# Performance work log

Measured on AMD Instinct MI355X. Metric: run time of the kernel, lower is better.

The kernel has to match this reference:

```python
import jax, jax.numpy as jnp
import numpy as np

IN_CH, OUT_CH = 256, 128
HID = 2 * OUT_CH  # 256
N_NODES, N_EDGES = 50000, 800000


def setup_inputs() -> dict:
    key = jax.random.key(0)
    k1, k2, k3, k4, k5, k6, k7 = jax.random.split(key, 7)
    feats = jax.random.normal(k1, (N_NODES, IN_CH), dtype=jnp.float32)
    src = jax.random.randint(k2, (N_EDGES,), 0, N_NODES, dtype=jnp.int64)
    dst = jax.random.randint(k3, (N_EDGES,), 0, N_NODES, dtype=jnp.int64)
    # GraphConv weights: layer0 in->2*out, layer1 2*out->out (Glorot-ish scale)
    W0 = jax.random.normal(k4, (IN_CH, HID), dtype=jnp.float32) / np.sqrt(IN_CH)
    b0 = jnp.zeros((HID,), dtype=jnp.float32)
    W1 = jax.random.normal(k5, (HID, OUT_CH), dtype=jnp.float32) / np.sqrt(HID)
    b1 = jnp.zeros((OUT_CH,), dtype=jnp.float32)
    return {"feats": feats, "src": src, "dst": dst, "W0": W0, "b0": b0, "W1": W1, "b1": b1}


def _graph_conv(x, W, b, src, dst, norm_src, norm_dst, n_nodes):
    # Apply W first (out <= in) to shrink the edge-gather intermediate, as DGL does.
    h = x @ W                                  # [N, out]
    h = h * norm_src[:, None]                  # D_src^-1/2
    msg = h[src]                               # [E, out] irregular gather
    agg = jax.ops.segment_sum(msg, dst, num_segments=n_nodes)  # SpMM
    agg = agg * norm_dst[:, None] + b          # D_dst^-1/2, bias
    return jax.nn.relu(agg)


def reference(feats, src, dst, W0, b0, W1, b1):
    n = feats.shape[0]
    loop = jnp.arange(n, dtype=src.dtype)
    src_sl = jnp.concatenate([src, loop])      # dgl.add_self_loop
    dst_sl = jnpp = jnp.concatenate([dst, loop])
    ones = jnp.ones_like(src_sl, dtype=feats.dtype)
    out_deg = jax.ops.segment_sum(ones, src_sl, num_segments=n)
    in_deg = jax.ops.segment_sum(ones, dst_sl, num_segments=n)
    norm_src = jax.lax.rsqrt(jnp.maximum(out_deg, 1.0))
    norm_dst = jax.lax.rsqrt(jnp.maximum(in_deg, 1.0))
    x = _graph_conv(feats, W0, b0, src_sl, dst_sl, norm_src, norm_dst, n)
    x = _graph_conv(x, W1, b1, src_sl, dst_sl, norm_src, norm_dst, n)
    return x
```

## Files before the change

kernel.cpp:

```cpp
#include <hip/hip_runtime.h>


typedef __attribute__((ext_vector_type(8))) short short8v;
typedef __attribute__((ext_vector_type(4))) float float4v;
typedef __attribute__((ext_vector_type(8))) _Float16 half8v;
typedef __attribute__((ext_vector_type(4))) _Float16 half4v;
typedef __attribute__((ext_vector_type(2))) _Float16 half2v;

__device__ inline unsigned short f2bf(float x) {
  unsigned u = __float_as_uint(x);
  return (unsigned short)((u + 0x7FFFu + ((u >> 16) & 1u)) >> 16);
}
__device__ inline float bf2f(unsigned short b) {
  return __uint_as_float(((unsigned)b) << 16);
}

__global__ __launch_bounds__(256) void k_hist8(const int* __restrict__ src,
                                               const int* __restrict__ dst,
                                               unsigned* __restrict__ cnt,
                                               int N, int E) {
  unsigned xcc;
  asm("s_getreg_b32 %0, hwreg(HW_REG_XCC_ID)" : "=s"(xcc));
  unsigned* my = cnt + (size_t)(xcc & 7) * 2u * (unsigned)N;
  int base = blockIdx.x * 1024 + threadIdx.x;
  int s4[4], d4[4];
  bool ok[4];
#pragma unroll
  for (int i = 0; i < 4; ++i) {
    int e = base + i * 256;
    ok[i] = e < E;
    if (ok[i]) { s4[i] = src[e]; d4[i] = dst[e]; }
  }
#pragma unroll
  for (int i = 0; i < 4; ++i) {
    if (ok[i]) {
      __hip_atomic_fetch_add(&my[s4[i]], 1u, __ATOMIC_RELAXED,
                             __HIP_MEMORY_SCOPE_WORKGROUP);
      __hip_atomic_fetch_add(&my[N + d4[i]], 1u, __ATOMIC_RELAXED,
                             __HIP_MEMORY_SCOPE_WORKGROUP);
    }
  }
}

__global__ __launch_bounds__(256) void k_scan1_norm(
    const unsigned* __restrict__ cnt, int* __restrict__ part,
    int* __restrict__ bsums, float* __restrict__ nsrc,
    float* __restrict__ ndst, int N) {
  __shared__ int s[256];
  int t = threadIdx.x, g = blockIdx.x * 256 + t;
  int od = 0, id = 0;
  if (g < N) {
#pragma unroll
    for (int x = 0; x < 8; ++x) {
      od += cnt[(size_t)x * 2u * (unsigned)N + g];
      id += cnt[(size_t)x * 2u * (unsigned)N + N + g];
    }
    nsrc[g] = rsqrtf((float)(od + 1));
    ndst[g] = rsqrtf((float)(id + 1));
  }
  int v = (g < N) ? id : 0;
  s[t] = v;
  __syncthreads();
  for (int o = 1; o < 256; o <<= 1) {
    int add = (t >= o) ? s[t - o] : 0;
    __syncthreads();
    s[t] += add;
    __syncthreads();
  }
  if (g < N) part[g] = s[t] - v;
  if (t == 255) bsums[blockIdx.x] = s[255];
}

__global__ __launch_bounds__(256) void k_scan23(
    int* __restrict__ part, int* __restrict__ cursor8,
    const int* __restrict__ bsums, const unsigned* __restrict__ cnt,
    int nb, int N, int E) {
  __shared__ int s[256];
  int t = threadIdx.x, g = blockIdx.x * 256 + t;
  int v = (t < nb) ? bsums[t] : 0;
  s[t] = v;
  __syncthreads();
  for (int o = 1; o < 256; o <<= 1) {
    int add = (t >= o) ? s[t - o] : 0;
    __syncthreads();
    s[t] += add;
    __syncthreads();
  }
  int off = s[blockIdx.x] - bsums[blockIdx.x];
  if (g < N) {
    int r = part[g] + off;
    part[g] = r;
    int run = r;
#pragma unroll
    for (int x = 0; x < 8; ++x) {
      cursor8[(size_t)x * N + g] = run;
      run += cnt[(size_t)x * 2u * (unsigned)N + N + g];
    }
  }
  if (g == 0) part[N] = E;
}

__global__ __launch_bounds__(256) void k_fill8(const int* __restrict__ src,
                                               const int* __restrict__ dst,
                                               int* __restrict__ cursor8,
                                               int* __restrict__ colidx,
                                               int N, int E) {
  unsigned xcc;
  asm("s_getreg_b32 %0, hwreg(HW_REG_XCC_ID)" : "=s"(xcc));
  int* my = cursor8 + (size_t)(xcc & 7) * N;
  int base = blockIdx.x * 1024 + threadIdx.x;
  int s4[4], d4[4];
  bool ok[4];
#pragma unroll
  for (int i = 0; i < 4; ++i) {
    int e = base + i * 256;
    ok[i] = e < E;
    if (ok[i]) { s4[i] = src[e]; d4[i] = dst[e]; }
  }
  int p4[4];
#pragma unroll
  for (int i = 0; i < 4; ++i) {
    if (ok[i])
      p4[i] = __hip_atomic_fetch_add(&my[d4[i]], 1, __ATOMIC_RELAXED,
                                     __HIP_MEMORY_SCOPE_WORKGROUP);
  }
#pragma unroll
  for (int i = 0; i < 4; ++i) {
    if (ok[i]) colidx[p4[i]] = s4[i];
  }
}

__global__ __launch_bounds__(256) void k_wsplit2(
    const float* __restrict__ W0, short* __restrict__ W0tH,
    short* __restrict__ W0tL, const float* __restrict__ W1,
    short* __restrict__ W1tH, short* __restrict__ W1tL) {
  const int K = 256, N0 = 256, N1 = 128;
  int idx = blockIdx.x * 256 + threadIdx.x;
  if (idx < K * N0) {
    int k = idx & (K - 1), n = idx >> 8;
    float v = W0[(size_t)k * N0 + n];
    unsigned short h = f2bf(v);
    W0tH[(size_t)n * K + k] = (short)h;
    W0tL[(size_t)n * K + k] = (short)f2bf(v - bf2f(h));
  } else {
    int j = idx - K * N0;
    if (j < K * N1) {
      int k = j & (K - 1), n = j >> 8;
      float v = W1[(size_t)k * N1 + n];
      unsigned short h = f2bf(v);
      W1tH[(size_t)n * K + k] = (short)h;
      W1tL[(size_t)n * K + k] = (short)f2bf(v - bf2f(h));
    }
  }
}

template <int NCOL, typename AT>
__global__ __launch_bounds__(256) void k_gemm_mfma(
    const AT* __restrict__ A, const short* __restrict__ WtH,
    const short* __restrict__ WtL, const float* __restrict__ norm,
    _Float16* __restrict__ out, int M) {
  constexpr int K = 256, BM = 64, BK = 32, PAD = 40, NF = NCOL / 16;
  __shared__ short AH[BM][PAD], AL[BM][PAD];
  __shared__ short BH[NCOL][PAD], BL[NCOL][PAD];
  int tid = threadIdx.x;
  int w = tid >> 6, l = tid & 63;
  int lg = l >> 4, ln = l & 15;
  int row0 = blockIdx.x * BM;

  float4v acc[NF];
#pragma unroll
  for (int i = 0; i < NF; ++i) acc[i] = (float4v){0.f, 0.f, 0.f, 0.f};

  int ar = tid >> 2;
  int akq = (tid & 3) * 8;

  for (int k0 = 0; k0 < K; k0 += BK) {
    float av[8];
    int grow = row0 + ar;
    if (grow < M) {
      if constexpr (sizeof(AT) == 4) {
        const float4* ap =
            reinterpret_cast<const float4*>(&A[(size_t)grow * K + k0 + akq]);
        float4 v0 = ap[0], v1 = ap[1];
        av[0] = v0.x; av[1] = v0.y; av[2] = v0.z; av[3] = v0.w;
        av[4] = v1.x; av[5] = v1.y; av[6] = v1.z; av[7] = v1.w;
      } else {
        half8v v =
            *reinterpret_cast<const half8v*>(&A[(size_t)grow * K + k0 + akq]);
#pragma unroll
        for (int i = 0; i < 8; ++i) av[i] = (float)v[i];
      }
    } else {
#pragma unroll
      for (int i = 0; i < 8; ++i) av[i] = 0.f;
    }
    short hh[8], ll[8];
#pragma unroll
    for (int i = 0; i < 8; ++i) {
      unsigned short h = f2bf(av[i]);
      hh[i] = (short)h;
      ll[i] = (short)f2bf(av[i] - bf2f(h));
    }
    *reinterpret_cast<short8v*>(&AH[ar][akq]) = *reinterpret_cast<short8v*>(hh);
    *reinterpret_cast<short8v*>(&AL[ar][akq]) = *reinterpret_cast<short8v*>(ll);

#pragma unroll
    for (int c = 0; c < NCOL / 64; ++c) {
      int chunk = c * 256 + tid;
      int bn = chunk >> 2, q = (chunk & 3) * 8;
      *reinterpret_cast<short8v*>(&BH[bn][q]) =
          *reinterpret_cast<const short8v*>(&WtH[(size_t)bn * K + k0 + q]);
      *reinterpret_cast<short8v*>(&BL[bn][q]) =
          *reinterpret_cast<const short8v*>(&WtL[(size_t)bn * K + k0 + q]);
    }
    __syncthreads();

    short8v aH = *reinterpret_cast<short8v*>(&AH[w * 16 + ln][lg * 8]);
    short8v aL = *reinterpret_cast<short8v*>(&AL[w * 16 + ln][lg * 8]);
#pragma unroll
    for (int nf = 0; nf < NF; ++nf) {
      short8v bHv = *reinterpret_cast<short8v*>(&BH[nf * 16 + ln][lg * 8]);
      short8v bLv = *reinterpret_cast<short8v*>(&BL[nf * 16 + ln][lg * 8]);
      acc[nf] = __builtin_amdgcn_mfma_f32_16x16x32_bf16(aH, bHv, acc[nf], 0, 0, 0);
      acc[nf] = __builtin_amdgcn_mfma_f32_16x16x32_bf16(aH, bLv, acc[nf], 0, 0, 0);
      acc[nf] = __builtin_amdgcn_mfma_f32_16x16x32_bf16(aL, bHv, acc[nf], 0, 0, 0);
    }
    __syncthreads();
  }

  int rbase = row0 + w * 16 + lg * 4;
  float nrm[4];
#pragma unroll
  for (int j = 0; j < 4; ++j)
    nrm[j] = (rbase + j < M) ? norm[rbase + j] : 0.f;
#pragma unroll
  for (int nf = 0; nf < NF; ++nf) {
#pragma unroll
    for (int j = 0; j < 4; ++j) {
      int r = rbase + j;
      if (r < M)
        out[(size_t)r * NCOL + nf * 16 + ln] = (_Float16)(acc[nf][j] * nrm[j]);
    }
  }
}

__global__ __launch_bounds__(256) void k_agg256(
    const _Float16* __restrict__ h, const int* __restrict__ rowptr,
    const int* __restrict__ colidx, const float* __restrict__ nd,
    const float* __restrict__ bias, _Float16* __restrict__ out, int N) {
  int node = blockIdx.x * 4 + (threadIdx.x >> 6);
  int lane = threadIdx.x & 63;
  if (node >= N) return;
  const half4v* hv = reinterpret_cast<const half4v*>(h);
  half4v hs = hv[(size_t)node * 64 + lane];
  float4 acc;
  acc.x = (float)hs[0]; acc.y = (float)hs[1];
  acc.z = (float)hs[2]; acc.w = (float)hs[3];
  int e0 = rowptr[node], e1 = rowptr[node + 1];
  int e = e0;
  for (; e + 7 < e1; e += 8) {
    int si[8];
#pragma unroll
    for (int i = 0; i < 8; ++i) si[i] = colidx[e + i];
    half4v v[8];
#pragma unroll
    for (int i = 0; i < 8; ++i) v[i] = hv[(size_t)si[i] * 64 + lane];
#pragma unroll
    for (int i = 0; i < 8; ++i) {
      acc.x += (float)v[i][0]; acc.y += (float)v[i][1];
      acc.z += (float)v[i][2]; acc.w += (float)v[i][3];
    }
  }
  for (; e < e1; ++e) {
    half4v v0 = hv[(size_t)colidx[e] * 64 + lane];
    acc.x += (float)v0[0]; acc.y += (float)v0[1];
    acc.z += (float)v0[2]; acc.w += (float)v0[3];
  }
  float n = nd[node];
  float4 b = reinterpret_cast<const float4*>(bias)[lane];
  half4v r = {(_Float16)fmaxf(fmaf(acc.x, n, b.x), 0.f),
              (_Float16)fmaxf(fmaf(acc.y, n, b.y), 0.f),
              (_Float16)fmaxf(fmaf(acc.z, n, b.z), 0.f),
              (_Float16)fmaxf(fmaf(acc.w, n, b.w), 0.f)};
  reinterpret_cast<half4v*>(out)[(size_t)node * 64 + lane] = r;
}

__global__ __launch_bounds__(256) void k_agg128(
    const _Float16* __restrict__ h, const int* __restrict__ rowptr,
    const int* __restrict__ colidx, const float* __restrict__ nd,
    const float* __restrict__ bias, float* __restrict__ out, int N) {
  int node = blockIdx.x * 4 + (threadIdx.x >> 6);
  int lane = threadIdx.x & 63;
  if (node >= N) return;
  const half2v* hv = reinterpret_cast<const half2v*>(h);
  half2v hs = hv[(size_t)node * 64 + lane];
  float2 acc;
  acc.x = (float)hs[0]; acc.y = (float)hs[1];
  int e0 = rowptr[node], e1 = rowptr[node + 1];
  int e = e0;
  for (; e + 7 < e1; e += 8) {
    int si[8];
#pragma unroll
    for (int i = 0; i < 8; ++i) si[i] = colidx[e + i];
    half2v v[8];
#pragma unroll
    for (int i = 0; i < 8; ++i) v[i] = hv[(size_t)si[i] * 64 + lane];
#pragma unroll
    for (int i = 0; i < 8; ++i) {
      acc.x += (float)v[i][0]; acc.y += (float)v[i][1];
    }
  }
  for (; e < e1; ++e) {
    half2v v0 = hv[(size_t)colidx[e] * 64 + lane];
    acc.x += (float)v0[0]; acc.y += (float)v0[1];
  }
  float n = nd[node];
  float2 b = reinterpret_cast<const float2*>(bias)[lane];
  float2 r;
  r.x = fmaxf(fmaf(acc.x, n, b.x), 0.f);
  r.y = fmaxf(fmaf(acc.y, n, b.y), 0.f);
  reinterpret_cast<float2*>(out)[(size_t)node * 64 + lane] = r;
}

extern "C" void kernel_launch(void* const* d_in, const int* in_sizes, int n_in,
                              void* d_out, int out_size, void* d_ws, size_t ws_size,
                              hipStream_t stream) {
  const float* feats = (const float*)d_in[0];
  const int* src = (const int*)d_in[1];
  const int* dst = (const int*)d_in[2];
  const float* W0 = (const float*)d_in[3];
  const float* b0 = (const float*)d_in[4];
  const float* W1 = (const float*)d_in[5];
  const float* b1 = (const float*)d_in[6];
  float* out = (float*)d_out;

  const int IN_CH = 256, HID = 256, OUT_CH = 128;
  int N = in_sizes[0] / IN_CH;
  int E = in_sizes[1];

  char* ws = (char*)d_ws;
  size_t off = 0;
  auto alloc = [&](size_t bytes) -> void* {
    void* p = ws + off;
    off += (bytes + 255) & ~(size_t)255;
    return p;
  };
  _Float16* h0 = (_Float16*)alloc((size_t)N * HID * 2);
  _Float16* x1 = (_Float16*)alloc((size_t)N * HID * 2);
  float* nsrc   = (float*)alloc((size_t)N * 4);
  float* ndst   = (float*)alloc((size_t)N * 4);
  unsigned* cnt = (unsigned*)alloc((size_t)8 * 2 * N * 4);
  int*   rowptr = (int*)alloc((size_t)(N + 1) * 4);
  int*  cursor8 = (int*)alloc((size_t)8 * N * 4);
  int*   colidx = (int*)alloc((size_t)E * 4);
  int*   bsums  = (int*)alloc(1024);
  short* w0h    = (short*)alloc((size_t)HID * IN_CH * 2);
  short* w0l    = (short*)alloc((size_t)HID * IN_CH * 2);
  short* w1h    = (short*)alloc((size_t)OUT_CH * HID * 2);
  short* w1l    = (short*)alloc((size_t)OUT_CH * HID * 2);
  _Float16* h1  = h0;

  hipMemsetAsync(cnt, 0, (size_t)8 * 2 * N * 4, stream);

  int nbE4 = (E + 1023) / 1024, nbN = (N + 255) / 256;
  k_hist8<<<nbE4, 256, 0, stream>>>(src, dst, cnt, N, E);
  k_scan1_norm<<<nbN, 256, 0, stream>>>(cnt, rowptr, bsums, nsrc, ndst, N);
  k_scan23<<<nbN, 256, 0, stream>>>(rowptr, cursor8, bsums, cnt, nbN, N, E);
  k_fill8<<<nbE4, 256, 0, stream>>>(src, dst, cursor8, colidx, N, E);

  k_wsplit2<<<(IN_CH * HID + HID * OUT_CH) / 256, 256, 0, stream>>>(
      W0, w0h, w0l, W1, w1h, w1l);

  int gm = (N + 63) / 64;
  k_gemm_mfma<256, float><<<gm, 256, 0, stream>>>(feats, w0h, w0l, nsrc, h0, N);
  k_agg256<<<(N + 3) / 4, 256, 0, stream>>>(h0, rowptr, colidx, ndst, b0, x1, N);

  k_gemm_mfma<128, _Float16><<<gm, 256, 0, stream>>>(x1, w1h, w1l, nsrc, h1, N);
  k_agg128<<<(N + 3) / 4, 256, 0, stream>>>(h1, rowptr, colidx, ndst, b1, out, N);
}
```

Baseline: 382.4 us.

## Build CSR with LDS-privatized histograms and fill over node slabs and edge chunks

Replaces the per-XCC global-atomic degree histogram and CSR fill with kernels that give each block a node slab (N/8 wide) and an edge chunk (E/32), counting and ranking with LDS atomics. Per-chunk count arrays replace the memset and make the fill deterministic within each chunk. The cost is that every block rescans its whole edge chunk for all 8 slabs, so src/dst are read 8 times. Only 256 blocks are launched, and the scan kernels now reduce over 32 chunk arrays instead of 8.

```diff
diff --git a/kernel.cpp b/kernel.cpp
--- a/kernel.cpp
+++ b/kernel.cpp
@@ -7,6 +7,10 @@
 typedef __attribute__((ext_vector_type(4))) _Float16 half4v;
 typedef __attribute__((ext_vector_type(2))) _Float16 half2v;
 
+#define NSLAB 8
+#define NCHUNK 32
+#define MAXW 6272
+
 __device__ inline unsigned short f2bf(float x) {
   unsigned u = __float_as_uint(x);
   return (unsigned short)((u + 0x7FFFu + ((u >> 16) & 1u)) >> 16);
@@ -15,45 +19,44 @@
   return __uint_as_float(((unsigned)b) << 16);
 }
 
-__global__ __launch_bounds__(256) void k_hist8(const int* __restrict__ src,
-                                               const int* __restrict__ dst,
-                                               unsigned* __restrict__ cnt,
-                                               int N, int E) {
-  unsigned xcc;
-  asm("s_getreg_b32 %0, hwreg(HW_REG_XCC_ID)" : "=s"(xcc));
-  unsigned* my = cnt + (size_t)(xcc & 7) * 2u * (unsigned)N;
-  int base = blockIdx.x * 1024 + threadIdx.x;
-  int s4[4], d4[4];
-  bool ok[4];
-#pragma unroll
-  for (int i = 0; i < 4; ++i) {
-    int e = base + i * 256;
-    ok[i] = e < E;
-    if (ok[i]) { s4[i] = src[e]; d4[i] = dst[e]; }
-  }
-#pragma unroll
-  for (int i = 0; i < 4; ++i) {
-    if (ok[i]) {
-      __hip_atomic_fetch_add(&my[s4[i]], 1u, __ATOMIC_RELAXED,
-                             __HIP_MEMORY_SCOPE_WORKGROUP);
-      __hip_atomic_fetch_add(&my[N + d4[i]], 1u, __ATOMIC_RELAXED,
-                             __HIP_MEMORY_SCOPE_WORKGROUP);
-    }
+__global__ __launch_bounds__(256) void k_histlds(
+    const int* __restrict__ src, const int* __restrict__ dst,
+    unsigned* __restrict__ cntO, unsigned* __restrict__ cntI,
+    int W, int CE, int N, int E) {
+  __shared__ unsigned ol[MAXW], il[MAXW];
+  int s = blockIdx.x & (NSLAB - 1), c = blockIdx.x >> 3;
+  int t = threadIdx.x;
+  for (int i = t; i < W; i += 256) { ol[i] = 0u; il[i] = 0u; }
+  __syncthreads();
+  int sW = s * W;
+  int e0 = c * CE, e1 = min(e0 + CE, E);
+  for (int e = e0 + t; e < e1; e += 256) {
+    int sv = src[e], dv = dst[e];
+    unsigned so = (unsigned)(sv - sW);
+    if (so < (unsigned)W) atomicAdd(&ol[so], 1u);
+    unsigned dof = (unsigned)(dv - sW);
+    if (dof < (unsigned)W) atomicAdd(&il[dof], 1u);
+  }
+  __syncthreads();
+  int hi = min(W, N - sW);
+  for (int i = t; i < hi; i += 256) {
+    cntO[(size_t)c * N + sW + i] = ol[i];
+    cntI[(size_t)c * N + sW + i] = il[i];
   }
 }
 
 __global__ __launch_bounds__(256) void k_scan1_norm(
-    const unsigned* __restrict__ cnt, int* __restrict__ part,
-    int* __restrict__ bsums, float* __restrict__ nsrc,
-    float* __restrict__ ndst, int N) {
+    const unsigned* __restrict__ cntO, const unsigned* __restrict__ cntI,
+    int* __restrict__ part, int* __restrict__ bsums,
+    float* __restrict__ nsrc, float* __restrict__ ndst, int N) {
   __shared__ int s[256];
   int t = threadIdx.x, g = blockIdx.x * 256 + t;
   int od = 0, id = 0;
   if (g < N) {
 #pragma unroll
-    for (int x = 0; x < 8; ++x) {
-      od += cnt[(size_t)x * 2u * (unsigned)N + g];
-      id += cnt[(size_t)x * 2u * (unsigned)N + N + g];
+    for (int c = 0; c < NCHUNK; ++c) {
+      od += cntO[(size_t)c * N + g];
+      id += cntI[(size_t)c * N + g];
     }
     nsrc[g] = rsqrtf((float)(od + 1));
     ndst[g] = rsqrtf((float)(id + 1));
@@ -72,8 +75,8 @@
 }
 
 __global__ __launch_bounds__(256) void k_scan23(
-    int* __restrict__ part, int* __restrict__ cursor8,
-    const int* __restrict__ bsums, const unsigned* __restrict__ cnt,
+    int* __restrict__ part, int* __restrict__ cursor32,
+    const int* __restrict__ bsums, const unsigned* __restrict__ cntI,
     int nb, int N, int E) {
   __shared__ int s[256];
   int t = threadIdx.x, g = blockIdx.x * 256 + t;
@@ -92,41 +95,33 @@
     part[g] = r;
     int run = r;
 #pragma unroll
-    for (int x = 0; x < 8; ++x) {
-      cursor8[(size_t)x * N + g] = run;
-      run += cnt[(size_t)x * 2u * (unsigned)N + N + g];
+    for (int c = 0; c < NCHUNK; ++c) {
+      cursor32[(size_t)c * N + g] = run;
+      run += cntI[(size_t)c * N + g];
     }
   }
   if (g == 0) part[N] = E;
 }
 
-__global__ __launch_bounds__(256) void k_fill8(const int* __restrict__ src,
-                                               const int* __restrict__ dst,
-                                               int* __restrict__ cursor8,
-                                               int* __restrict__ colidx,
-                                               int N, int E) {
-  unsigned xcc;
-  asm("s_getreg_b32 %0, hwreg(HW_REG_XCC_ID)" : "=s"(xcc));
-  int* my = cursor8 + (size_t)(xcc & 7) * N;
-  int base = blockIdx.x * 1024 + threadIdx.x;
-  int s4[4], d4[4];
-  bool ok[4];
-#pragma unroll
-  for (int i = 0; i < 4; ++i) {
-    int e = base + i * 256;
-    ok[i] = e < E;
-    if (ok[i]) { s4[i] = src[e]; d4[i] = dst[e]; }
-  }
-  int p4[4];
-#pragma unroll
-  for (int i = 0; i < 4; ++i) {
-    if (ok[i])
-      p4[i] = __hip_atomic_fetch_add(&my[d4[i]], 1, __ATOMIC_RELAXED,
-                                     __HIP_MEMORY_SCOPE_WORKGROUP);
-  }
-#pragma unroll
-  for (int i = 0; i < 4; ++i) {
-    if (ok[i]) colidx[p4[i]] = s4[i];
+__global__ __launch_bounds__(256) void k_fill_lds(
+    const int* __restrict__ src, const int* __restrict__ dst,
+    const int* __restrict__ cursor32, int* __restrict__ colidx,
+    int W, int CE, int N, int E) {
+  __shared__ unsigned rl[MAXW];
+  int s = blockIdx.x & (NSLAB - 1), c = blockIdx.x >> 3;
+  int t = threadIdx.x;
+  for (int i = t; i < W; i += 256) rl[i] = 0u;
+  __syncthreads();
+  int sW = s * W;
+  int e0 = c * CE, e1 = min(e0 + CE, E);
+  const int* cbase = cursor32 + (size_t)c * N;
+  for (int e = e0 + t; e < e1; e += 256) {
+    int sv = src[e], dv = dst[e];
+    unsigned dof = (unsigned)(dv - sW);
+    if (dof < (unsigned)W) {
+      unsigned r = atomicAdd(&rl[dof], 1u);
+      colidx[cbase[dv] + (int)r] = sv;
+    }
   }
 }
 
@@ -337,6 +332,8 @@
   const int IN_CH = 256, HID = 256, OUT_CH = 128;
   int N = in_sizes[0] / IN_CH;
   int E = in_sizes[1];
+  int W = (N + NSLAB - 1) / NSLAB;
+  int CE = (E + NCHUNK - 1) / NCHUNK;
 
   char* ws = (char*)d_ws;
   size_t off = 0;
@@ -349,9 +346,10 @@
   _Float16* x1 = (_Float16*)alloc((size_t)N * HID * 2);
   float* nsrc   = (float*)alloc((size_t)N * 4);
   float* ndst   = (float*)alloc((size_t)N * 4);
-  unsigned* cnt = (unsigned*)alloc((size_t)8 * 2 * N * 4);
+  unsigned* cntO = (unsigned*)alloc((size_t)NCHUNK * N * 4);
+  unsigned* cntI = (unsigned*)alloc((size_t)NCHUNK * N * 4);
   int*   rowptr = (int*)alloc((size_t)(N + 1) * 4);
-  int*  cursor8 = (int*)alloc((size_t)8 * N * 4);
+  int* cursor32 = (int*)alloc((size_t)NCHUNK * N * 4);
   int*   colidx = (int*)alloc((size_t)E * 4);
   int*   bsums  = (int*)alloc(1024);
   short* w0h    = (short*)alloc((size_t)HID * IN_CH * 2);
@@ -360,13 +358,11 @@
   short* w1l    = (short*)alloc((size_t)OUT_CH * HID * 2);
   _Float16* h1  = h0;
 
-  hipMemsetAsync(cnt, 0, (size_t)8 * 2 * N * 4, stream);
-
-  int nbE4 = (E + 1023) / 1024, nbN = (N + 255) / 256;
-  k_hist8<<<nbE4, 256, 0, stream>>>(src, dst, cnt, N, E);
-  k_scan1_norm<<<nbN, 256, 0, stream>>>(cnt, rowptr, bsums, nsrc, ndst, N);
-  k_scan23<<<nbN, 256, 0, stream>>>(rowptr, cursor8, bsums, cnt, nbN, N, E);
-  k_fill8<<<nbE4, 256, 0, stream>>>(src, dst, cursor8, colidx, N, E);
+  int nbN = (N + 255) / 256;
+  k_histlds<<<NSLAB * NCHUNK, 256, 0, stream>>>(src, dst, cntO, cntI, W, CE, N, E);
+  k_scan1_norm<<<nbN, 256, 0, stream>>>(cntO, cntI, rowptr, bsums, nsrc, ndst, N);
+  k_scan23<<<nbN, 256, 0, stream>>>(rowptr, cursor32, bsums, cntI, nbN, N, E);
+  k_fill_lds<<<NSLAB * NCHUNK, 256, 0, stream>>>(src, dst, cursor32, colidx, W, CE, N, E);
 
   k_wsplit2<<<(IN_CH * HID + HID * OUT_CH) / 256, 256, 0, stream>>>(
       W0, w0h, w0l, W1, w1h, w1l);
```

Measured after the change: 377.0 us. No clear change (-1.4%).
